# Optimization experiments

Measured on AMD Instinct MI355X. Metric: run time of the kernel, lower is better.

## Reference

```python
import jax, jax.numpy as jnp
import numpy as np

N, E, F0, H = 100000, 3200000, 256, 128
TEMP = 2.0
ALPHA = 0.2  # leaky relu slope
EPS_BN = 1e-5
EPS_LN = 1e-5


def spmm(vals, row, col, X):
    # sparse [N,N] @ dense [N,D] via gather + segment_sum
    return jax.ops.segment_sum(vals[:, None] * X[col], row, num_segments=N)


def batchnorm(h, g, b):
    mu = jnp.mean(h, axis=0, keepdims=True)
    var = jnp.var(h, axis=0, keepdims=True)
    return (h - mu) * jax.lax.rsqrt(var + EPS_BN) * g + b


def layernorm(h, g, b):
    mu = jnp.mean(h, axis=-1, keepdims=True)
    var = jnp.var(h, axis=-1, keepdims=True)
    return (h - mu) * jax.lax.rsqrt(var + EPS_LN) * g + b


def setup_inputs() -> dict:
    key = jax.random.key(0)
    ks = jax.random.split(key, 32)
    x = jax.random.normal(ks[0], (N, F0), dtype=jnp.float32)
    edge_row = jax.random.randint(ks[1], (E,), 0, N)
    edge_col = jax.random.randint(ks[2], (E,), 0, N)
    adj_vals = jax.random.uniform(ks[3], (E,), dtype=jnp.float32) / 32.0  # ~normalized adj
    sf = lambda k, sh: jax.random.normal(k, sh, dtype=jnp.float32) * 0.05
    in_dim = 3 * F0 + 1
    return {
        "x": x, "edge_row": edge_row, "edge_col": edge_col, "adj_vals": adj_vals,
        # LowPassExtractor (GCN)
        "W_gc1": sf(ks[4], (F0, 2 * H)), "b_gc1": jnp.zeros((2 * H,), jnp.float32),
        "bn1_g": jnp.ones((2 * H,), jnp.float32), "bn1_b": jnp.zeros((2 * H,), jnp.float32),
        "W_gc2": sf(ks[5], (2 * H, H)), "b_gc2": jnp.zeros((H,), jnp.float32),
        "bn2_g": jnp.ones((H,), jnp.float32), "bn2_b": jnp.zeros((H,), jnp.float32),
        # Gating
        "Wg1": sf(ks[6], (in_dim, H)), "bg1": jnp.zeros((H,), jnp.float32),
        "ln_g": jnp.ones((H,), jnp.float32), "ln_b": jnp.zeros((H,), jnp.float32),
        "Wg2": sf(ks[7], (H, 2)), "bg2": jnp.zeros((2,), jnp.float32),
        # HighPassExpert
        "Wxp": sf(ks[8], (F0, H)), "bxp": jnp.zeros((H,), jnp.float32),
        "res_scale": jnp.asarray(1.0, jnp.float32),
        "rn_g": jnp.ones((H,), jnp.float32), "rn_b": jnp.zeros((H,), jnp.float32),
        "Wq": sf(ks[9], (H, H)), "Wk": sf(ks[10], (H, H)), "Wv": sf(ks[11], (H, H)),
    }


def reference(x, edge_row, edge_col, adj_vals,
              W_gc1, b_gc1, bn1_g, bn1_b, W_gc2, b_gc2, bn2_g, bn2_b,
              Wg1, bg1, ln_g, ln_b, Wg2, bg2,
              Wxp, bxp, res_scale, rn_g, rn_b, Wq, Wk, Wv):
    # ---- LowPassExtractor: two GCN layers (spmm(adj, xW)+b) with batchnorm+relu
    h1 = jax.nn.relu(batchnorm(spmm(adj_vals, edge_row, edge_col, x @ W_gc1) + b_gc1, bn1_g, bn1_b))
    low = jax.nn.relu(batchnorm(spmm(adj_vals, edge_row, edge_col, h1 @ W_gc2) + b_gc2, bn2_g, bn2_b))

    # ---- Gating: neighborhood stats via spmm
    AX = spmm(adj_vals, edge_row, edge_col, x)
    deg = jax.ops.segment_sum(adj_vals, edge_row, num_segments=N)[:, None]
    x_mean = AX / (deg + 1e-8)
    AX2 = spmm(adj_vals, edge_row, edge_col, x * x)
    var = AX2 / (deg + 1e-8) - x_mean * x_mean
    x_std = jnp.sqrt(jnp.clip(var, 0.0))
    x_cat = jnp.concatenate([x, AX - x, x_std, deg], axis=1)  # [N, 3*F0+1]
    hg = jax.nn.relu(layernorm(x_cat @ Wg1 + bg1, ln_g, ln_b))
    gate = jax.nn.softmax((hg @ Wg2 + bg2) / TEMP, axis=1)  # [N, 2]

    # ---- HighPassExpert: GAT-style sparse attention on normalized residual
    residual = layernorm(res_scale * (x @ Wxp + bxp - low), rn_g, rn_b)
    Q, K, V = residual @ Wq, residual @ Wk, residual @ Wv
    scores = jnp.sum(Q[edge_row] * K[edge_col], axis=1) / jnp.sqrt(jnp.float32(H))
    exp_s = jnp.exp(jnp.where(scores > 0, scores, ALPHA * scores))
    denom = jax.ops.segment_sum(exp_s, edge_row, num_segments=N)
    attn = exp_s / (denom[edge_row] + 1e-16)
    high = jax.ops.segment_sum(attn[:, None] * V[edge_col], edge_row, num_segments=N)

    output = gate[:, 0:1] * low + gate[:, 1:2] * high
    return output, gate, low, high
```

## Files before the change

kernel.cpp:

```cpp
#include <hip/hip_runtime.h>

#define F0 256
#define HD 128
#define NP 100352

typedef unsigned short u16;
typedef __attribute__((ext_vector_type(8))) short short8;
typedef __attribute__((ext_vector_type(4))) float f32x4;

__device__ inline float bf2f(u16 u) {
    union { unsigned int i; float f; } v; v.i = ((unsigned int)u) << 16; return v.f;
}
__device__ inline u16 f2bf(float f) {
    union { float f; unsigned int i; } v; v.f = f;
    unsigned int r = v.i + 0x7FFF + ((v.i >> 16) & 1);
    return (u16)(r >> 16);
}

#define GLOAD16(gp, lp) __builtin_amdgcn_global_load_lds( \
    (const __attribute__((address_space(1))) void*)(gp), \
    (__attribute__((address_space(3))) void*)(lp), 16, 0, 0)

__global__ void k_hist(const int* __restrict__ row, int* __restrict__ counts, int E) {
    int e = blockIdx.x * blockDim.x + threadIdx.x;
    if (e < E) atomicAdd(&counts[row[e]], 1);
}

__global__ void k_scan_blk(const int* __restrict__ counts, int* __restrict__ scan_out,
                           int* __restrict__ partials, int n) {
    __shared__ int wsum[16];
    int t = threadIdx.x;
    int i = blockIdx.x * 1024 + t;
    int v = (i < n) ? counts[i] : 0;
    int lane = t & 63, w = t >> 6;
    #pragma unroll
    for (int off = 1; off < 64; off <<= 1) { int u = __shfl_up(v, off); if (lane >= off) v += u; }
    if (lane == 63) wsum[w] = v;
    __syncthreads();
    if (t < 16) {
        int s = wsum[t];
        #pragma unroll
        for (int off = 1; off < 16; off <<= 1) { int u = __shfl_up(s, off); if (t >= off) s += u; }
        wsum[t] = s;
    }
    __syncthreads();
    int add = (w > 0) ? wsum[w - 1] : 0;
    if (i < n) scan_out[i] = v + add;
    if (t == 1023) partials[blockIdx.x] = wsum[15];
}

__global__ void k_scan_part(int* partials, int nb) {
    __shared__ int ws2[2];
    int t = threadIdx.x;
    int v = (t < nb) ? partials[t] : 0;
    int lane = t & 63, w = t >> 6;
    #pragma unroll
    for (int off = 1; off < 64; off <<= 1) { int u = __shfl_up(v, off); if (lane >= off) v += u; }
    if (lane == 63) ws2[w] = v;
    __syncthreads();
    if (w == 1) v += ws2[0];
    if (t < nb) partials[t] = v;
}

__global__ void k_scan_add(int* __restrict__ row_ptr, const int* __restrict__ partials, int n) {
    int b = blockIdx.x;
    int i = b * 1024 + threadIdx.x;
    if (b == 0 && threadIdx.x == 0) row_ptr[0] = 0;
    int add = (b > 0) ? partials[b - 1] : 0;
    if (i < n) row_ptr[1 + i] += add;
}

__global__ void k_binit(const int* __restrict__ row_ptr, int* __restrict__ bcursor, int nb) {
    int b = blockIdx.x * 256 + threadIdx.x;
    if (b < nb) bcursor[b] = row_ptr[b << 10];
}

__global__ __launch_bounds__(256) void k_bucketA(const int* __restrict__ erow,
                                                 const int* __restrict__ ecol,
                                                 const float* __restrict__ avals,
                                                 int* __restrict__ bcursor,
                                                 int4* __restrict__ tmp, int E, int nb) {
    __shared__ int hcnt[128];
    __shared__ int hbase[128];
    int t = threadIdx.x;
    for (int i = t; i < nb; i += 256) hcnt[i] = 0;
    __syncthreads();
    int start = blockIdx.x * 2048;
    int r[8], c[8]; float v[8]; int loc[8];
    #pragma unroll
    for (int k = 0; k < 8; ++k) {
        int e = start + k * 256 + t;
        bool ok = e < E;
        r[k] = ok ? erow[e] : -1;
        c[k] = ok ? ecol[e] : 0;
        v[k] = ok ? avals[e] : 0.f;
        loc[k] = (r[k] >= 0) ? atomicAdd(&hcnt[r[k] >> 10], 1) : 0;
    }
    __syncthreads();
    for (int i = t; i < nb; i += 256) hbase[i] = atomicAdd(&bcursor[i], hcnt[i]);
    __syncthreads();
    #pragma unroll
    for (int k = 0; k < 8; ++k) {
        if (r[k] >= 0) {
            int b = r[k] >> 10;
            tmp[(size_t)hbase[b] + loc[k]] = make_int4(r[k], c[k], __float_as_int(v[k]), 0);
        }
    }
}

__global__ void k_bucketB(const int4* __restrict__ tmp, const int* __restrict__ row_ptr,
                          int* __restrict__ cursor, int2* __restrict__ cv, int E) {
    for (int e = blockIdx.x * 256 + threadIdx.x; e < E; e += gridDim.x * 256) {
        int4 tt = tmp[e];
        int pos = row_ptr[tt.x] + atomicAdd(&cursor[tt.x], 1);
        cv[pos] = make_int2(tt.y, tt.z);
    }
}

__global__ void k_cast_x(const float* __restrict__ x, u16* __restrict__ xb, int total4) {
    int i = blockIdx.x * blockDim.x + threadIdx.x;
    if (i >= total4) return;
    float4 v = ((const float4*)x)[i];
    ((ushort4*)xb)[i] = make_ushort4(f2bf(v.x), f2bf(v.y), f2bf(v.z), f2bf(v.w));
}

__global__ void k_prep_w(const float* __restrict__ W_gc1, const float* __restrict__ W_gc2,
                         const float* __restrict__ Wg1, const float* __restrict__ Wxp,
                         const float* __restrict__ Wq, const float* __restrict__ Wk,
                         const float* __restrict__ Wv,
                         u16* Wgc1t, u16* Wgc2t, u16* Wdt, u16* W1t, u16* W2t,
                         u16* Wxpt, u16* Wqt, u16* Wkt, u16* Wvt) {
    int z = blockIdx.z;
    int idx = blockIdx.x * 256 + threadIdx.x;
    if (z == 0) { if (idx < 65536) { int n = idx >> 8, k = idx & 255; Wgc1t[idx] = f2bf(W_gc1[k * 256 + n]); } }
    else if (z == 1) { if (idx < 32768) { int n = idx >> 8, k = idx & 255; Wgc2t[idx] = f2bf(W_gc2[k * 128 + n]); } }
    else if (z == 2) { if (idx < 32768) { int n = idx >> 8, k = idx & 255; Wdt[idx] = f2bf(Wg1[k * 128 + n] - Wg1[(k + 256) * 128 + n]); } }
    else if (z == 3) { if (idx < 32768) { int n = idx >> 8, k = idx & 255; W1t[idx] = f2bf(Wg1[(k + 256) * 128 + n]); } }
    else if (z == 4) { if (idx < 32768) { int n = idx >> 8, k = idx & 255; W2t[idx] = f2bf(Wg1[(k + 512) * 128 + n]); } }
    else if (z == 5) { if (idx < 32768) { int n = idx >> 8, k = idx & 255; Wxpt[idx] = f2bf(Wxp[k * 128 + n]); } }
    else if (z == 6) { if (idx < 16384) { int n = idx >> 7, k = idx & 127; Wqt[idx] = f2bf(Wq[k * 128 + n]); } }
    else if (z == 7) { if (idx < 16384) { int n = idx >> 7, k = idx & 127; Wkt[idx] = f2bf(Wk[k * 128 + n]); } }
    else if (z == 8) { if (idx < 16384) { int n = idx >> 7, k = idx & 127; Wvt[idx] = f2bf(Wv[k * 128 + n]); } }
}

__global__ void k_spmm_x2(const u16* __restrict__ Xb, const int* __restrict__ row_ptr,
                          const int2* __restrict__ cv,
                          u16* __restrict__ AXb, u16* __restrict__ XSTDb,
                          float* __restrict__ deg, int N) {
    int wid = blockIdx.x * 4 + (threadIdx.x >> 6);
    if (wid >= N) return;
    int lane = threadIdx.x & 63;
    float a0 = 0, a1 = 0, a2 = 0, a3 = 0;
    float q0 = 0, q1 = 0, q2 = 0, q3 = 0, d = 0;
    int s = row_ptr[wid], e = row_ptr[wid + 1];
    int j = s;
    for (; j + 3 < e; j += 4) {
        int2 cc[4]; ushort4 xb[4];
        #pragma unroll
        for (int t = 0; t < 4; ++t) cc[t] = cv[j + t];
        #pragma unroll
        for (int t = 0; t < 4; ++t) xb[t] = *(const ushort4*)(Xb + (size_t)cc[t].x * F0 + lane * 4);
        #pragma unroll
        for (int t = 0; t < 4; ++t) {
            float x0 = bf2f(xb[t].x), x1 = bf2f(xb[t].y), x2 = bf2f(xb[t].z), x3 = bf2f(xb[t].w);
            float vv = __int_as_float(cc[t].y);
            a0 += vv * x0; a1 += vv * x1; a2 += vv * x2; a3 += vv * x3;
            q0 += vv * x0 * x0; q1 += vv * x1 * x1; q2 += vv * x2 * x2; q3 += vv * x3 * x3;
            d += vv;
        }
    }
    for (; j < e; ++j) {
        int2 cc = cv[j];
        float v0 = __int_as_float(cc.y);
        ushort4 xb0 = *(const ushort4*)(Xb + (size_t)cc.x * F0 + lane * 4);
        float x0 = bf2f(xb0.x), x1 = bf2f(xb0.y), x2 = bf2f(xb0.z), x3 = bf2f(xb0.w);
        a0 += v0 * x0; a1 += v0 * x1; a2 += v0 * x2; a3 += v0 * x3;
        q0 += v0 * x0 * x0; q1 += v0 * x1 * x1; q2 += v0 * x2 * x2; q3 += v0 * x3 * x3;
        d += v0;
    }
    float inv = 1.0f / (d + 1e-8f);
    float m0 = a0 * inv, m1 = a1 * inv, m2 = a2 * inv, m3 = a3 * inv;
    float s0 = sqrtf(fmaxf(q0 * inv - m0 * m0, 0.f));
    float s1 = sqrtf(fmaxf(q1 * inv - m1 * m1, 0.f));
    float s2 = sqrtf(fmaxf(q2 * inv - m2 * m2, 0.f));
    float s3 = sqrtf(fmaxf(q3 * inv - m3 * m3, 0.f));
    *(ushort4*)(AXb + (size_t)wid * F0 + lane * 4) = make_ushort4(f2bf(a0), f2bf(a1), f2bf(a2), f2bf(a3));
    *(ushort4*)(XSTDb + (size_t)wid * F0 + lane * 4) = make_ushort4(f2bf(s0), f2bf(s1), f2bf(s2), f2bf(s3));
    if (lane == 0) deg[wid] = d;
}

__global__ void k_spmm128(const u16* __restrict__ Xb, const int* __restrict__ row_ptr,
                          const int2* __restrict__ cv, u16* __restrict__ OUT, int N) {
    int wid = blockIdx.x * 4 + (threadIdx.x >> 6);
    if (wid >= N) return;
    int lane = threadIdx.x & 63;
    float a0 = 0, a1 = 0;
    int s = row_ptr[wid], e = row_ptr[wid + 1];
    int j = s;
    for (; j + 3 < e; j += 4) {
        int2 cc[4]; ushort2 xb[4];
        #pragma unroll
        for (int t = 0; t < 4; ++t) cc[t] = cv[j + t];
        #pragma unroll
        for (int t = 0; t < 4; ++t) xb[t] = *(const ushort2*)(Xb + (size_t)cc[t].x * HD + lane * 2);
        #pragma unroll
        for (int t = 0; t < 4; ++t) {
            float vv = __int_as_float(cc[t].y);
            a0 += vv * bf2f(xb[t].x); a1 += vv * bf2f(xb[t].y);
        }
    }
    for (; j < e; ++j) {
        int2 cc = cv[j];
        float v0 = __int_as_float(cc.y);
        ushort2 x0 = *(const ushort2*)(Xb + (size_t)cc.x * HD + lane * 2);
        a0 += v0 * bf2f(x0.x); a1 += v0 * bf2f(x0.y);
    }
    *(ushort2*)(OUT + (size_t)wid * HD + lane * 2) = make_ushort2(f2bf(a0), f2bf(a1));
}

__device__ inline void mm_core(const u16* __restrict__ A, const u16* __restrict__ Bt,
                               int K, int ldA, int ldB, int m0, int n0,
                               u16* As, u16* Bs, f32x4 acc[4][4]) {
    int t = threadIdx.x, w = t >> 6, l = t & 63;
    int wr = (w >> 1) * 64, wc = (w & 1) * 64;
    int aoff = (wr + (l & 15)) * 32 + (l >> 4) * 8;
    int boff = (wc + (l & 15)) * 32 + (l >> 4) * 8;
    for (int k0 = 0; k0 < K; k0 += 32) {
        __syncthreads();
        #pragma unroll
        for (int s = 0; s < 2; ++s) {
            int i = s * 256 + t;
            int row = i >> 2, ch = i & 3;
            GLOAD16(A + (size_t)(m0 + row) * ldA + k0 + ch * 8, As + i * 8);
            GLOAD16(Bt + (size_t)(n0 + row) * ldB + k0 + ch * 8, Bs + i * 8);
        }
        __syncthreads();
        short8 af[4], bfr[4];
        #pragma unroll
        for (int i = 0; i < 4; ++i) af[i] = *(const short8*)(As + aoff + i * 16 * 32);
        #pragma unroll
        for (int j = 0; j < 4; ++j) bfr[j] = *(const short8*)(Bs + boff + j * 16 * 32);
        #pragma unroll
        for (int i = 0; i < 4; ++i)
            #pragma unroll
            for (int j = 0; j < 4; ++j)
                acc[i][j] = __builtin_amdgcn_mfma_f32_16x16x32_bf16(af[i], bfr[j], acc[i][j], 0, 0, 0);
    }
}

__device__ inline void mm_zero(f32x4 acc[4][4]) {
    #pragma unroll
    for (int i = 0; i < 4; ++i)
        #pragma unroll
        for (int j = 0; j < 4; ++j)
            acc[i][j] = (f32x4){0.f, 0.f, 0.f, 0.f};
}

__global__ __launch_bounds__(256) void k_mm_f32(const u16* __restrict__ A, const u16* __restrict__ Bt,
                                                float* __restrict__ C, const float* __restrict__ bias,
                                                int M, int K, int Nc) {
    __shared__ __align__(16) u16 As[128 * 32];
    __shared__ __align__(16) u16 Bs[128 * 32];
    int m0 = blockIdx.x * 128, n0 = blockIdx.y * 128;
    f32x4 acc[4][4]; mm_zero(acc);
    mm_core(A, Bt, K, K, K, m0, n0, As, Bs, acc);
    int t = threadIdx.x, w = t >> 6, l = t & 63;
    int rbase = m0 + (w >> 1) * 64 + (l >> 4) * 4;
    int cbase = n0 + (w & 1) * 64 + (l & 15);
    #pragma unroll
    for (int j = 0; j < 4; ++j) {
        float bj = bias ? bias[cbase + j * 16] : 0.f;
        #pragma unroll
        for (int i = 0; i < 4; ++i)
            #pragma unroll
            for (int r = 0; r < 4; ++r) {
                int row = rbase + i * 16 + r;
                if (row < M) C[(size_t)row * Nc + cbase + j * 16] = acc[i][j][r] + bj;
            }
    }
}

__global__ __launch_bounds__(256) void k_mm_bf(const u16* __restrict__ A, const u16* __restrict__ Bt,
                                               u16* __restrict__ C, int M, int K, int Nc) {
    __shared__ __align__(16) u16 As[128 * 32];
    __shared__ __align__(16) u16 Bs[128 * 32];
    int m0 = blockIdx.x * 128, n0 = blockIdx.y * 128;
    f32x4 acc[4][4]; mm_zero(acc);
    mm_core(A, Bt, K, K, K, m0, n0, As, Bs, acc);
    int t = threadIdx.x, w = t >> 6, l = t & 63;
    int rbase = m0 + (w >> 1) * 64 + (l >> 4) * 4;
    int cbase = n0 + (w & 1) * 64 + (l & 15);
    #pragma unroll
    for (int j = 0; j < 4; ++j)
        #pragma unroll
        for (int i = 0; i < 4; ++i)
            #pragma unroll
            for (int r = 0; r < 4; ++r) {
                int row = rbase + i * 16 + r;
                if (row < M) C[(size_t)row * Nc + cbase + j * 16] = f2bf(acc[i][j][r]);
            }
}

__global__ __launch_bounds__(256) void k_mm_gate(const u16* A0, const u16* A1, const u16* A2,
                                                 const u16* B0, const u16* B1, const u16* B2,
                                                 float* __restrict__ C, const float* __restrict__ bg1,
                                                 const float* __restrict__ wlast,
                                                 const float* __restrict__ deg, int M) {
    __shared__ __align__(16) u16 As[128 * 32];
    __shared__ __align__(16) u16 Bs[128 * 32];
    int m0 = blockIdx.x * 128;
    f32x4 acc[4][4]; mm_zero(acc);
    mm_core(A0, B0, 256, 256, 256, m0, 0, As, Bs, acc);
    mm_core(A1, B1, 256, 256, 256, m0, 0, As, Bs, acc);
    mm_core(A2, B2, 256, 256, 256, m0, 0, As, Bs, acc);
    int t = threadIdx.x, w = t >> 6, l = t & 63;
    int rbase = m0 + (w >> 1) * 64 + (l >> 4) * 4;
    int cbase = (w & 1) * 64 + (l & 15);
    float wl[4], bg[4];
    #pragma unroll
    for (int j = 0; j < 4; ++j) { wl[j] = wlast[cbase + j * 16]; bg[j] = bg1[cbase + j * 16]; }
    float dg[4][4];
    #pragma unroll
    for (int i = 0; i < 4; ++i)
        #pragma unroll
        for (int r = 0; r < 4; ++r) {
            int row = rbase + i * 16 + r;
            dg[i][r] = (row < M) ? deg[row] : 0.f;
        }
    #pragma unroll
    for (int j = 0; j < 4; ++j)
        #pragma unroll
        for (int i = 0; i < 4; ++i)
            #pragma unroll
            for (int r = 0; r < 4; ++r) {
                int row = rbase + i * 16 + r;
                if (row < M) C[(size_t)row * 128 + cbase + j * 16] = acc[i][j][r] + bg[j] + dg[i][r] * wl[j];
            }
}

__global__ __launch_bounds__(256) void k_mm_qkv(const u16* __restrict__ A,
                                                const u16* Wqt, const u16* Wkt, const u16* Wvt,
                                                float* Q, u16* Kb, u16* Vb, int M) {
    __shared__ __align__(16) u16 As[128 * 32];
    __shared__ __align__(16) u16 Bs[128 * 32];
    int z = blockIdx.z;
    const u16* Bt = (z == 0) ? Wqt : (z == 1) ? Wkt : Wvt;
    int m0 = blockIdx.x * 128;
    f32x4 acc[4][4]; mm_zero(acc);
    mm_core(A, Bt, 128, 128, 128, m0, 0, As, Bs, acc);
    int t = threadIdx.x, w = t >> 6, l = t & 63;
    int rbase = m0 + (w >> 1) * 64 + (l >> 4) * 4;
    int cbase = (w & 1) * 64 + (l & 15);
    if (z == 0) {
        #pragma unroll
        for (int j = 0; j < 4; ++j)
            #pragma unroll
            for (int i = 0; i < 4; ++i)
                #pragma unroll
                for (int r = 0; r < 4; ++r) {
                    int row = rbase + i * 16 + r;
                    if (row < M) Q[(size_t)row * 128 + cbase + j * 16] = acc[i][j][r];
                }
    } else {
        u16* C = (z == 1) ? Kb : Vb;
        #pragma unroll
        for (int j = 0; j < 4; ++j)
            #pragma unroll
            for (int i = 0; i < 4; ++i)
                #pragma unroll
                for (int r = 0; r < 4; ++r) {
                    int row = rbase + i * 16 + r;
                    if (row < M) C[(size_t)row * 128 + cbase + j * 16] = f2bf(acc[i][j][r]);
                }
    }
}

__global__ void k_bn_stats_bf(const u16* __restrict__ H, double* __restrict__ stats, int N, int C) {
    int t = threadIdx.x;
    int rpt = 256 / C;
    int rsub = t / C;
    int col = t - rsub * C;
    double s = 0.0, q = 0.0;
    for (long r = (long)blockIdx.x * rpt + rsub; r < N; r += (long)gridDim.x * rpt) {
        float v = bf2f(H[(size_t)r * C + col]);
        s += v; q += (double)v * v;
    }
    __shared__ double sh_s[256], sh_q[256];
    sh_s[t] = s; sh_q[t] = q;
    __syncthreads();
    if (t < C) {
        for (int k = 1; k < rpt; ++k) { s += sh_s[t + k * C]; q += sh_q[t + k * C]; }
        atomicAdd(&stats[t], s);
        atomicAdd(&stats[C + t], q);
    }
}

__global__ void k_bn_fin(const double* __restrict__ stats, const float* __restrict__ g,
                         const float* __restrict__ b, float* __restrict__ scale,
                         float* __restrict__ shift, int C, double invN) {
    int t = threadIdx.x;
    if (t >= C) return;
    double mean = stats[t] * invN;
    double var = stats[C + t] * invN - mean * mean;
    float sc = (float)((double)g[t] / sqrt(var + 1e-5));
    scale[t] = sc;
    shift[t] = b[t] - (float)mean * sc;
}

__global__ void k_bn_relu_bb(const u16* __restrict__ in, u16* __restrict__ out,
                             const float* __restrict__ scale, const float* __restrict__ shift,
                             int total4, int cmask4) {
    int i = blockIdx.x * blockDim.x + threadIdx.x;
    if (i >= total4) return;
    int c4 = i & cmask4;
    ushort4 v = ((const ushort4*)in)[i];
    float4 sc = ((const float4*)scale)[c4];
    float4 sh = ((const float4*)shift)[c4];
    ((ushort4*)out)[i] = make_ushort4(
        f2bf(fmaxf(bf2f(v.x) * sc.x + sh.x, 0.f)), f2bf(fmaxf(bf2f(v.y) * sc.y + sh.y, 0.f)),
        f2bf(fmaxf(bf2f(v.z) * sc.z + sh.z, 0.f)), f2bf(fmaxf(bf2f(v.w) * sc.w + sh.w, 0.f)));
}

__global__ void k_bn_relu_bf(const u16* __restrict__ in, float* __restrict__ out,
                             const float* __restrict__ scale, const float* __restrict__ shift,
                             int total4, int cmask4) {
    int i = blockIdx.x * blockDim.x + threadIdx.x;
    if (i >= total4) return;
    int c4 = i & cmask4;
    ushort4 v = ((const ushort4*)in)[i];
    float4 sc = ((const float4*)scale)[c4];
    float4 sh = ((const float4*)shift)[c4];
    ((float4*)out)[i] = make_float4(
        fmaxf(bf2f(v.x) * sc.x + sh.x, 0.f), fmaxf(bf2f(v.y) * sc.y + sh.y, 0.f),
        fmaxf(bf2f(v.z) * sc.z + sh.z, 0.f), fmaxf(bf2f(v.w) * sc.w + sh.w, 0.f));
}

__global__ void k_ln_gate(const float* __restrict__ Hg, const float* __restrict__ g,
                          const float* __restrict__ b, const float* __restrict__ Wg2,
                          const float* __restrict__ bg2, float* __restrict__ gate, int N) {
    int wid = blockIdx.x * 4 + (threadIdx.x >> 6);
    if (wid >= N) return;
    int lane = threadIdx.x & 63;
    float2 h = *(const float2*)(Hg + (size_t)wid * HD + lane * 2);
    float s1 = h.x + h.y, s2 = h.x * h.x + h.y * h.y;
    #pragma unroll
    for (int off = 32; off > 0; off >>= 1) { s1 += __shfl_xor(s1, off); s2 += __shfl_xor(s2, off); }
    float mu = s1 * (1.f / 128.f);
    float var = s2 * (1.f / 128.f) - mu * mu;
    float is = 1.0f / sqrtf(var + 1e-5f);
    float2 gg = *(const float2*)(g + lane * 2);
    float2 bb = *(const float2*)(b + lane * 2);
    float y0 = fmaxf((h.x - mu) * is * gg.x + bb.x, 0.f);
    float y1 = fmaxf((h.y - mu) * is * gg.y + bb.y, 0.f);
    float4 w = ((const float4*)Wg2)[lane];
    float t0 = y0 * w.x + y1 * w.z;
    float t1 = y0 * w.y + y1 * w.w;
    #pragma unroll
    for (int off = 32; off > 0; off >>= 1) { t0 += __shfl_xor(t0, off); t1 += __shfl_xor(t1, off); }
    if (lane == 0) {
        t0 = (t0 + bg2[0]) * 0.5f;
        t1 = (t1 + bg2[1]) * 0.5f;
        float m = fmaxf(t0, t1);
        float e0 = __expf(t0 - m), e1 = __expf(t1 - m);
        float inv = 1.0f / (e0 + e1);
        gate[(size_t)wid * 2 + 0] = e0 * inv;
        gate[(size_t)wid * 2 + 1] = e1 * inv;
    }
}

__global__ void k_resid_ln(const float* __restrict__ R0, const float* __restrict__ low,
                           const float* __restrict__ g, const float* __restrict__ b,
                           const float* __restrict__ rs_ptr, u16* __restrict__ resid, int N) {
    int wid = blockIdx.x * 4 + (threadIdx.x >> 6);
    if (wid >= N) return;
    int lane = threadIdx.x & 63;
    float rs = rs_ptr[0];
    float2 a = *(const float2*)(R0 + (size_t)wid * HD + lane * 2);
    float2 l = *(const float2*)(low + (size_t)wid * HD + lane * 2);
    float h0 = rs * (a.x - l.x), h1 = rs * (a.y - l.y);
    float s1 = h0 + h1, s2 = h0 * h0 + h1 * h1;
    #pragma unroll
    for (int off = 32; off > 0; off >>= 1) { s1 += __shfl_xor(s1, off); s2 += __shfl_xor(s2, off); }
    float mu = s1 * (1.f / 128.f);
    float var = s2 * (1.f / 128.f) - mu * mu;
    float is = 1.0f / sqrtf(var + 1e-5f);
    float2 gg = *(const float2*)(g + lane * 2);
    float2 bb = *(const float2*)(b + lane * 2);
    float y0 = (h0 - mu) * is * gg.x + bb.x;
    float y1 = (h1 - mu) * is * gg.y + bb.y;
    *(ushort2*)(resid + (size_t)wid * HD + lane * 2) = make_ushort2(f2bf(y0), f2bf(y1));
}

__global__ void k_attn_aggr(const float* __restrict__ Q, const u16* __restrict__ Kb,
                            const u16* __restrict__ Vb, const int* __restrict__ row_ptr,
                            const int2* __restrict__ cv,
                            const float* __restrict__ gate, const float* __restrict__ low,
                            float* __restrict__ high, float* __restrict__ outp, int N) {
    int wid = blockIdx.x * 4 + (threadIdx.x >> 6);
    if (wid >= N) return;
    int lane = threadIdx.x & 63;
    int sub = lane & 15;
    int g = lane >> 4;
    float qs[8];
    {
        const float4* qp = (const float4*)(Q + (size_t)wid * HD + sub * 8);
        float4 q0 = qp[0], q1 = qp[1];
        qs[0] = q0.x; qs[1] = q0.y; qs[2] = q0.z; qs[3] = q0.w;
        qs[4] = q1.x; qs[5] = q1.y; qs[6] = q1.z; qs[7] = q1.w;
    }
    float2 qv = *(const float2*)(Q + (size_t)wid * HD + lane * 2);
    float n0 = 0, n1 = 0, den = 0;
    int s = row_ptr[wid], e = row_ptr[wid + 1];
    int j = s;
    for (; j + 3 < e; j += 4) {
        int cg = cv[j + g].x;
        short8 kk = *(const short8*)(Kb + (size_t)cg * HD + sub * 8);
        float p = qs[0] * bf2f((u16)kk[0]) + qs[1] * bf2f((u16)kk[1])
                + qs[2] * bf2f((u16)kk[2]) + qs[3] * bf2f((u16)kk[3])
                + qs[4] * bf2f((u16)kk[4]) + qs[5] * bf2f((u16)kk[5])
                + qs[6] * bf2f((u16)kk[6]) + qs[7] * bf2f((u16)kk[7]);
        p += __shfl_xor(p, 1); p += __shfl_xor(p, 2);
        p += __shfl_xor(p, 4); p += __shfl_xor(p, 8);
        float sc = p * 0.08838834764831845f;
        float ls = sc > 0.f ? sc : 0.2f * sc;
        float ex = __expf(ls);
        float exb[4]; int cb[4];
        #pragma unroll
        for (int t = 0; t < 4; ++t) { exb[t] = __shfl(ex, t << 4); cb[t] = __shfl(cg, t << 4); }
        ushort2 vb[4];
        #pragma unroll
        for (int t = 0; t < 4; ++t) vb[t] = *(const ushort2*)(Vb + (size_t)cb[t] * HD + lane * 2);
        #pragma unroll
        for (int t = 0; t < 4; ++t) {
            n0 += exb[t] * bf2f(vb[t].x);
            n1 += exb[t] * bf2f(vb[t].y);
            den += exb[t];
        }
    }
    for (; j < e; ++j) {
        int c0 = cv[j].x;
        ushort2 kb0 = *(const ushort2*)(Kb + (size_t)c0 * HD + lane * 2);
        ushort2 vb0 = *(const ushort2*)(Vb + (size_t)c0 * HD + lane * 2);
        float sc0 = qv.x * bf2f(kb0.x) + qv.y * bf2f(kb0.y);
        #pragma unroll
        for (int off = 32; off > 0; off >>= 1) sc0 += __shfl_xor(sc0, off);
        float p = sc0 * 0.08838834764831845f;
        float ls = p > 0.f ? p : 0.2f * p;
        float ex = __expf(ls);
        n0 += ex * bf2f(vb0.x); n1 += ex * bf2f(vb0.y); den += ex;
    }
    float inv = 1.0f / (den + 1e-16f);
    float h0 = n0 * inv, h1 = n1 * inv;
    *(float2*)(high + (size_t)wid * HD + lane * 2) = make_float2(h0, h1);
    float g0 = gate[(size_t)wid * 2 + 0], g1 = gate[(size_t)wid * 2 + 1];
    float2 lw = *(const float2*)(low + (size_t)wid * HD + lane * 2);
    *(float2*)(outp + (size_t)wid * HD + lane * 2) = make_float2(g0 * lw.x + g1 * h0, g0 * lw.y + g1 * h1);
}

extern "C" void kernel_launch(void* const* d_in, const int* in_sizes, int n_in,
                              void* d_out, int out_size, void* d_ws, size_t ws_size,
                              hipStream_t stream) {
    const float* x      = (const float*)d_in[0];
    const int*   erow   = (const int*)d_in[1];
    const int*   ecol   = (const int*)d_in[2];
    const float* avals  = (const float*)d_in[3];
    const float* W_gc1  = (const float*)d_in[4];
    const float* bn1_g  = (const float*)d_in[6];
    const float* bn1_b  = (const float*)d_in[7];
    const float* W_gc2  = (const float*)d_in[8];
    const float* bn2_g  = (const float*)d_in[10];
    const float* bn2_b  = (const float*)d_in[11];
    const float* Wg1    = (const float*)d_in[12];
    const float* bg1    = (const float*)d_in[13];
    const float* ln_g   = (const float*)d_in[14];
    const float* ln_b   = (const float*)d_in[15];
    const float* Wg2    = (const float*)d_in[16];
    const float* bg2    = (const float*)d_in[17];
    const float* Wxp    = (const float*)d_in[18];
    const float* bxp    = (const float*)d_in[19];
    const float* rscale = (const float*)d_in[20];
    const float* rn_g   = (const float*)d_in[21];
    const float* rn_b   = (const float*)d_in[22];
    const float* Wq     = (const float*)d_in[23];
    const float* Wk     = (const float*)d_in[24];
    const float* Wv     = (const float*)d_in[25];

    const int N = in_sizes[0] / F0;
    const int E = in_sizes[1];

    char* base = (char*)d_ws;
    size_t off = 0;
    auto carve = [&](size_t bytes) -> char* {
        char* p = base + off;
        off += (bytes + 255) & ~(size_t)255;
        return p;
    };
    double* stats  = (double*)carve(4096);
    float* scaleb  = (float*)carve(1024);
    float* shiftb  = (float*)carve(1024);
    int*   partials= (int*)carve(2048);
    int*   bcursor = (int*)carve(512);
    u16* Wgc1t = (u16*)carve(65536 * 2);
    u16* Wgc2t = (u16*)carve(32768 * 2);
    u16* Wdt   = (u16*)carve(32768 * 2);
    u16* W1t   = (u16*)carve(32768 * 2);
    u16* W2t   = (u16*)carve(32768 * 2);
    u16* Wxpt  = (u16*)carve(32768 * 2);
    u16* Wqt   = (u16*)carve(16384 * 2);
    u16* Wkt   = (u16*)carve(16384 * 2);
    u16* Wvt   = (u16*)carve(16384 * 2);
    int*   row_ptr = (int*)carve((size_t)(N + 1) * 4);
    int*   cursor  = (int*)carve((size_t)N * 4);
    float* deg     = (float*)carve((size_t)N * 4);
    int2*  cv      = (int2*)carve((size_t)E * 8);
    u16*   x_bf    = (u16*)carve((size_t)NP * F0 * 2);
    u16*   kvb     = (u16*)carve((size_t)NP * HD * 2 * 2);
    u16*   AX_bf   = (u16*)carve((size_t)NP * F0 * 2);
    u16*   XSTD_bf = (u16*)carve((size_t)NP * F0 * 2);
    u16*   h1_bf   = (u16*)carve((size_t)NP * F0 * 2);
    float* BIG3    = (float*)carve((size_t)NP * HD * 4);
    u16*   G2_bf   = (u16*)carve((size_t)NP * HD * 2);
    float* M3      = (float*)carve((size_t)NP * HD * 4);
    (void)ws_size; (void)n_in; (void)out_size;

    u16*   Kb    = kvb;
    u16*   Vb    = kvb + (size_t)N * HD;
    u16*   S1_bf = h1_bf;
    u16*   S2_bf = (u16*)BIG3;
    u16*   resid_bf = h1_bf;
    int4*  tmp   = (int4*)M3;

    float* out_o    = (float*)d_out;
    float* out_gate = out_o + (size_t)N * HD;
    float* out_low  = out_gate + (size_t)N * 2;
    float* out_high = out_low + (size_t)N * HD;

    const int eb  = (E + 255) / 256;
    const int wb  = (N + 3) / 4;
    const int NB1 = (N + 1023) / 1024;
    const int nb  = (N + 1023) >> 10;
    const int gx  = (N + 127) / 128;
    const dim3 blk(256);

    hipMemsetAsync(cursor, 0, (size_t)N * 4, stream);
    k_hist<<<eb, blk, 0, stream>>>(erow, cursor, E);
    k_scan_blk<<<NB1, 1024, 0, stream>>>(cursor, row_ptr + 1, partials, N);
    k_scan_part<<<1, 128, 0, stream>>>(partials, NB1);
    k_scan_add<<<NB1, 1024, 0, stream>>>(row_ptr, partials, N);
    k_binit<<<1, blk, 0, stream>>>(row_ptr, bcursor, nb);
    k_bucketA<<<(E + 2047) / 2048, blk, 0, stream>>>(erow, ecol, avals, bcursor, tmp, E, nb);
    hipMemsetAsync(cursor, 0, (size_t)N * 4, stream);
    k_bucketB<<<2048, blk, 0, stream>>>(tmp, row_ptr, cursor, cv, E);

    k_cast_x<<<(N * 64 + 255) / 256, blk, 0, stream>>>(x, x_bf, N * 64);
    k_prep_w<<<dim3(256, 1, 9), blk, 0, stream>>>(W_gc1, W_gc2, Wg1, Wxp, Wq, Wk, Wv,
                                                  Wgc1t, Wgc2t, Wdt, W1t, W2t, Wxpt, Wqt, Wkt, Wvt);

    k_spmm_x2<<<wb, blk, 0, stream>>>(x_bf, row_ptr, cv, AX_bf, XSTD_bf, deg, N);

    k_mm_bf<<<dim3(gx, 2), blk, 0, stream>>>(AX_bf, Wgc1t, S1_bf, N, 256, 256);
    hipMemsetAsync(stats, 0, 4096, stream);
    k_bn_stats_bf<<<1024, blk, 0, stream>>>(S1_bf, stats, N, 256);
    k_bn_fin<<<1, blk, 0, stream>>>(stats, bn1_g, bn1_b, scaleb, shiftb, 256, 1.0 / N);
    k_bn_relu_bb<<<(N * 64 + 255) / 256, blk, 0, stream>>>(S1_bf, h1_bf, scaleb, shiftb, N * 64, 63);
    k_mm_bf<<<dim3(gx, 1), blk, 0, stream>>>(h1_bf, Wgc2t, G2_bf, N, 256, 128);
    k_spmm128<<<wb, blk, 0, stream>>>(G2_bf, row_ptr, cv, S2_bf, N);
    hipMemsetAsync(stats, 0, 2048, stream);
    k_bn_stats_bf<<<1024, blk, 0, stream>>>(S2_bf, stats, N, 128);
    k_bn_fin<<<1, blk, 0, stream>>>(stats, bn2_g, bn2_b, scaleb, shiftb, 128, 1.0 / N);
    k_bn_relu_bf<<<(N * 32 + 255) / 256, blk, 0, stream>>>(S2_bf, out_low, scaleb, shiftb, N * 32, 31);

    k_mm_gate<<<dim3(gx, 1), blk, 0, stream>>>(x_bf, AX_bf, XSTD_bf, Wdt, W1t, W2t,
                                               M3, bg1, Wg1 + (size_t)768 * 128, deg, N);
    k_ln_gate<<<wb, blk, 0, stream>>>(M3, ln_g, ln_b, Wg2, bg2, out_gate, N);

    k_mm_f32<<<dim3(gx, 1), blk, 0, stream>>>(x_bf, Wxpt, BIG3, bxp, N, 256, 128);
    k_resid_ln<<<wb, blk, 0, stream>>>(BIG3, out_low, rn_g, rn_b, rscale, resid_bf, N);
    k_mm_qkv<<<dim3(gx, 1, 3), blk, 0, stream>>>(resid_bf, Wqt, Wkt, Wvt, M3, Kb, Vb, N);
    k_attn_aggr<<<wb, blk, 0, stream>>>(M3, Kb, Vb, row_ptr, cv, out_gate, out_low, out_high, out_o, N);
}
```

Baseline: 1.549 ms.

## Simplify CSR build via atomic ranks, unroll gathers by 8, interleave K/V

The histogram kernel now records each edge's atomic rank, so a single direct scatter kernel replaces the two-pass bucketed CSR construction and its extra memset. The SpMM and attention-aggregation kernels add an 8-edge unrolled loop to keep more gathers in flight. K and V are stored interleaved per node in one 256-wide row, so both come from the same region of memory. The direct scatter writes to random positions in cv, losing the locality that bucketing provided, and the wider unroll raises register pressure.

```diff
diff --git a/kernel.cpp b/kernel.cpp
--- a/kernel.cpp
+++ b/kernel.cpp
@@ -21,9 +21,10 @@
     (const __attribute__((address_space(1))) void*)(gp), \
     (__attribute__((address_space(3))) void*)(lp), 16, 0, 0)
 
-__global__ void k_hist(const int* __restrict__ row, int* __restrict__ counts, int E) {
+__global__ void k_hist_rank(const int* __restrict__ row, int* __restrict__ counts,
+                            int* __restrict__ rank, int E) {
     int e = blockIdx.x * blockDim.x + threadIdx.x;
-    if (e < E) atomicAdd(&counts[row[e]], 1);
+    if (e < E) rank[e] = atomicAdd(&counts[row[e]], 1);
 }
 
 __global__ void k_scan_blk(const int* __restrict__ counts, int* __restrict__ scan_out,
@@ -70,51 +71,14 @@
     if (i < n) row_ptr[1 + i] += add;
 }
 
-__global__ void k_binit(const int* __restrict__ row_ptr, int* __restrict__ bcursor, int nb) {
-    int b = blockIdx.x * 256 + threadIdx.x;
-    if (b < nb) bcursor[b] = row_ptr[b << 10];
-}
-
-__global__ __launch_bounds__(256) void k_bucketA(const int* __restrict__ erow,
-                                                 const int* __restrict__ ecol,
-                                                 const float* __restrict__ avals,
-                                                 int* __restrict__ bcursor,
-                                                 int4* __restrict__ tmp, int E, int nb) {
-    __shared__ int hcnt[128];
-    __shared__ int hbase[128];
-    int t = threadIdx.x;
-    for (int i = t; i < nb; i += 256) hcnt[i] = 0;
-    __syncthreads();
-    int start = blockIdx.x * 2048;
-    int r[8], c[8]; float v[8]; int loc[8];
-    #pragma unroll
-    for (int k = 0; k < 8; ++k) {
-        int e = start + k * 256 + t;
-        bool ok = e < E;
-        r[k] = ok ? erow[e] : -1;
-        c[k] = ok ? ecol[e] : 0;
-        v[k] = ok ? avals[e] : 0.f;
-        loc[k] = (r[k] >= 0) ? atomicAdd(&hcnt[r[k] >> 10], 1) : 0;
-    }
-    __syncthreads();
-    for (int i = t; i < nb; i += 256) hbase[i] = atomicAdd(&bcursor[i], hcnt[i]);
-    __syncthreads();
-    #pragma unroll
-    for (int k = 0; k < 8; ++k) {
-        if (r[k] >= 0) {
-            int b = r[k] >> 10;
-            tmp[(size_t)hbase[b] + loc[k]] = make_int4(r[k], c[k], __float_as_int(v[k]), 0);
-        }
-    }
-}
-
-__global__ void k_bucketB(const int4* __restrict__ tmp, const int* __restrict__ row_ptr,
-                          int* __restrict__ cursor, int2* __restrict__ cv, int E) {
-    for (int e = blockIdx.x * 256 + threadIdx.x; e < E; e += gridDim.x * 256) {
-        int4 tt = tmp[e];
-        int pos = row_ptr[tt.x] + atomicAdd(&cursor[tt.x], 1);
-        cv[pos] = make_int2(tt.y, tt.z);
-    }
+__global__ void k_scatter_direct(const int* __restrict__ row, const int* __restrict__ ecol,
+                                 const float* __restrict__ avals, const int* __restrict__ rank,
+                                 const int* __restrict__ row_ptr, int2* __restrict__ cv, int E) {
+    int e = blockIdx.x * blockDim.x + threadIdx.x;
+    if (e >= E) return;
+    int r = row[e];
+    int pos = row_ptr[r] + rank[e];
+    cv[pos] = make_int2(ecol[e], __float_as_int(avals[e]));
 }
 
 __global__ void k_cast_x(const float* __restrict__ x, u16* __restrict__ xb, int total4) {
@@ -154,6 +118,21 @@
     float q0 = 0, q1 = 0, q2 = 0, q3 = 0, d = 0;
     int s = row_ptr[wid], e = row_ptr[wid + 1];
     int j = s;
+    for (; j + 7 < e; j += 8) {
+        int2 cc[8]; ushort4 xb[8];
+        #pragma unroll
+        for (int t = 0; t < 8; ++t) cc[t] = cv[j + t];
+        #pragma unroll
+        for (int t = 0; t < 8; ++t) xb[t] = *(const ushort4*)(Xb + (size_t)cc[t].x * F0 + lane * 4);
+        #pragma unroll
+        for (int t = 0; t < 8; ++t) {
+            float x0 = bf2f(xb[t].x), x1 = bf2f(xb[t].y), x2 = bf2f(xb[t].z), x3 = bf2f(xb[t].w);
+            float vv = __int_as_float(cc[t].y);
+            a0 += vv * x0; a1 += vv * x1; a2 += vv * x2; a3 += vv * x3;
+            q0 += vv * x0 * x0; q1 += vv * x1 * x1; q2 += vv * x2 * x2; q3 += vv * x3 * x3;
+            d += vv;
+        }
+    }
     for (; j + 3 < e; j += 4) {
         int2 cc[4]; ushort4 xb[4];
         #pragma unroll
@@ -197,6 +176,18 @@
     float a0 = 0, a1 = 0;
     int s = row_ptr[wid], e = row_ptr[wid + 1];
     int j = s;
+    for (; j + 7 < e; j += 8) {
+        int2 cc[8]; ushort2 xb[8];
+        #pragma unroll
+        for (int t = 0; t < 8; ++t) cc[t] = cv[j + t];
+        #pragma unroll
+        for (int t = 0; t < 8; ++t) xb[t] = *(const ushort2*)(Xb + (size_t)cc[t].x * HD + lane * 2);
+        #pragma unroll
+        for (int t = 0; t < 8; ++t) {
+            float vv = __int_as_float(cc[t].y);
+            a0 += vv * bf2f(xb[t].x); a1 += vv * bf2f(xb[t].y);
+        }
+    }
     for (; j + 3 < e; j += 4) {
         int2 cc[4]; ushort2 xb[4];
         #pragma unroll
@@ -340,7 +331,7 @@
 
 __global__ __launch_bounds__(256) void k_mm_qkv(const u16* __restrict__ A,
                                                 const u16* Wqt, const u16* Wkt, const u16* Wvt,
-                                                float* Q, u16* Kb, u16* Vb, int M) {
+                                                float* Q, u16* KV, int M) {
     __shared__ __align__(16) u16 As[128 * 32];
     __shared__ __align__(16) u16 Bs[128 * 32];
     int z = blockIdx.z;
@@ -362,7 +353,7 @@
                     if (row < M) Q[(size_t)row * 128 + cbase + j * 16] = acc[i][j][r];
                 }
     } else {
-        u16* C = (z == 1) ? Kb : Vb;
+        int coff = (z == 1) ? 0 : 128;
         #pragma unroll
         for (int j = 0; j < 4; ++j)
             #pragma unroll
@@ -370,7 +361,7 @@
                 #pragma unroll
                 for (int r = 0; r < 4; ++r) {
                     int row = rbase + i * 16 + r;
-                    if (row < M) C[(size_t)row * 128 + cbase + j * 16] = f2bf(acc[i][j][r]);
+                    if (row < M) KV[(size_t)row * 256 + coff + cbase + j * 16] = f2bf(acc[i][j][r]);
                 }
     }
 }
@@ -491,9 +482,8 @@
     *(ushort2*)(resid + (size_t)wid * HD + lane * 2) = make_ushort2(f2bf(y0), f2bf(y1));
 }
 
-__global__ void k_attn_aggr(const float* __restrict__ Q, const u16* __restrict__ Kb,
-                            const u16* __restrict__ Vb, const int* __restrict__ row_ptr,
-                            const int2* __restrict__ cv,
+__global__ void k_attn_aggr(const float* __restrict__ Q, const u16* __restrict__ KV,
+                            const int* __restrict__ row_ptr, const int2* __restrict__ cv,
                             const float* __restrict__ gate, const float* __restrict__ low,
                             float* __restrict__ high, float* __restrict__ outp, int N) {
     int wid = blockIdx.x * 4 + (threadIdx.x >> 6);
@@ -512,9 +502,48 @@
     float n0 = 0, n1 = 0, den = 0;
     int s = row_ptr[wid], e = row_ptr[wid + 1];
     int j = s;
+    for (; j + 7 < e; j += 8) {
+        int cg0 = cv[j + g].x;
+        int cg1 = cv[j + 4 + g].x;
+        short8 ka = *(const short8*)(KV + (size_t)cg0 * 256 + sub * 8);
+        short8 kb = *(const short8*)(KV + (size_t)cg1 * 256 + sub * 8);
+        float p0 = qs[0] * bf2f((u16)ka[0]) + qs[1] * bf2f((u16)ka[1])
+                 + qs[2] * bf2f((u16)ka[2]) + qs[3] * bf2f((u16)ka[3])
+                 + qs[4] * bf2f((u16)ka[4]) + qs[5] * bf2f((u16)ka[5])
+                 + qs[6] * bf2f((u16)ka[6]) + qs[7] * bf2f((u16)ka[7]);
+        float p1 = qs[0] * bf2f((u16)kb[0]) + qs[1] * bf2f((u16)kb[1])
+                 + qs[2] * bf2f((u16)kb[2]) + qs[3] * bf2f((u16)kb[3])
+                 + qs[4] * bf2f((u16)kb[4]) + qs[5] * bf2f((u16)kb[5])
+                 + qs[6] * bf2f((u16)kb[6]) + qs[7] * bf2f((u16)kb[7]);
+        p0 += __shfl_xor(p0, 1); p1 += __shfl_xor(p1, 1);
+        p0 += __shfl_xor(p0, 2); p1 += __shfl_xor(p1, 2);
+        p0 += __shfl_xor(p0, 4); p1 += __shfl_xor(p1, 4);
+        p0 += __shfl_xor(p0, 8); p1 += __shfl_xor(p1, 8);
+        float sc0 = p0 * 0.08838834764831845f;
+        float sc1 = p1 * 0.08838834764831845f;
+        float ls0 = sc0 > 0.f ? sc0 : 0.2f * sc0;
+        float ls1 = sc1 > 0.f ? sc1 : 0.2f * sc1;
+        float ex0 = __expf(ls0);
+        float ex1 = __expf(ls1);
+        float exb[8]; int cb[8];
+        #pragma unroll
+        for (int t = 0; t < 4; ++t) {
+            exb[t]     = __shfl(ex0, t << 4); cb[t]     = __shfl(cg0, t << 4);
+            exb[4 + t] = __shfl(ex1, t << 4); cb[4 + t] = __shfl(cg1, t << 4);
+        }
+        ushort2 vb[8];
+        #pragma unroll
+        for (int t = 0; t < 8; ++t) vb[t] = *(const ushort2*)(KV + (size_t)cb[t] * 256 + 128 + lane * 2);
+        #pragma unroll
+        for (int t = 0; t < 8; ++t) {
+            n0 += exb[t] * bf2f(vb[t].x);
+            n1 += exb[t] * bf2f(vb[t].y);
+            den += exb[t];
+        }
+    }
     for (; j + 3 < e; j += 4) {
         int cg = cv[j + g].x;
-        short8 kk = *(const short8*)(Kb + (size_t)cg * HD + sub * 8);
+        short8 kk = *(const short8*)(KV + (size_t)cg * 256 + sub * 8);
         float p = qs[0] * bf2f((u16)kk[0]) + qs[1] * bf2f((u16)kk[1])
                 + qs[2] * bf2f((u16)kk[2]) + qs[3] * bf2f((u16)kk[3])
                 + qs[4] * bf2f((u16)kk[4]) + qs[5] * bf2f((u16)kk[5])
@@ -529,7 +558,7 @@
         for (int t = 0; t < 4; ++t) { exb[t] = __shfl(ex, t << 4); cb[t] = __shfl(cg, t << 4); }
         ushort2 vb[4];
         #pragma unroll
-        for (int t = 0; t < 4; ++t) vb[t] = *(const ushort2*)(Vb + (size_t)cb[t] * HD + lane * 2);
+        for (int t = 0; t < 4; ++t) vb[t] = *(const ushort2*)(KV + (size_t)cb[t] * 256 + 128 + lane * 2);
         #pragma unroll
         for (int t = 0; t < 4; ++t) {
             n0 += exb[t] * bf2f(vb[t].x);
@@ -539,8 +568,8 @@
     }
     for (; j < e; ++j) {
         int c0 = cv[j].x;
-        ushort2 kb0 = *(const ushort2*)(Kb + (size_t)c0 * HD + lane * 2);
-        ushort2 vb0 = *(const ushort2*)(Vb + (size_t)c0 * HD + lane * 2);
+        ushort2 kb0 = *(const ushort2*)(KV + (size_t)c0 * 256 + lane * 2);
+        ushort2 vb0 = *(const ushort2*)(KV + (size_t)c0 * 256 + 128 + lane * 2);
         float sc0 = qv.x * bf2f(kb0.x) + qv.y * bf2f(kb0.y);
         #pragma unroll
         for (int off = 32; off > 0; off >>= 1) sc0 += __shfl_xor(sc0, off);
@@ -599,7 +628,6 @@
     float* scaleb  = (float*)carve(1024);
     float* shiftb  = (float*)carve(1024);
     int*   partials= (int*)carve(2048);
-    int*   bcursor = (int*)carve(512);
     u16* Wgc1t = (u16*)carve(65536 * 2);
     u16* Wgc2t = (u16*)carve(32768 * 2);
     u16* Wdt   = (u16*)carve(32768 * 2);
@@ -614,7 +642,7 @@
     float* deg     = (float*)carve((size_t)N * 4);
     int2*  cv      = (int2*)carve((size_t)E * 8);
     u16*   x_bf    = (u16*)carve((size_t)NP * F0 * 2);
-    u16*   kvb     = (u16*)carve((size_t)NP * HD * 2 * 2);
+    u16*   kvb     = (u16*)carve((size_t)NP * 256 * 2);
     u16*   AX_bf   = (u16*)carve((size_t)NP * F0 * 2);
     u16*   XSTD_bf = (u16*)carve((size_t)NP * F0 * 2);
     u16*   h1_bf   = (u16*)carve((size_t)NP * F0 * 2);
@@ -623,12 +651,10 @@
     float* M3      = (float*)carve((size_t)NP * HD * 4);
     (void)ws_size; (void)n_in; (void)out_size;
 
-    u16*   Kb    = kvb;
-    u16*   Vb    = kvb + (size_t)N * HD;
     u16*   S1_bf = h1_bf;
     u16*   S2_bf = (u16*)BIG3;
     u16*   resid_bf = h1_bf;
-    int4*  tmp   = (int4*)M3;
+    int*   rank  = (int*)M3;
 
     float* out_o    = (float*)d_out;
     float* out_gate = out_o + (size_t)N * HD;
@@ -638,19 +664,15 @@
     const int eb  = (E + 255) / 256;
     const int wb  = (N + 3) / 4;
     const int NB1 = (N + 1023) / 1024;
-    const int nb  = (N + 1023) >> 10;
     const int gx  = (N + 127) / 128;
     const dim3 blk(256);
 
     hipMemsetAsync(cursor, 0, (size_t)N * 4, stream);
-    k_hist<<<eb, blk, 0, stream>>>(erow, cursor, E);
+    k_hist_rank<<<eb, blk, 0, stream>>>(erow, cursor, rank, E);
     k_scan_blk<<<NB1, 1024, 0, stream>>>(cursor, row_ptr + 1, partials, N);
     k_scan_part<<<1, 128, 0, stream>>>(partials, NB1);
     k_scan_add<<<NB1, 1024, 0, stream>>>(row_ptr, partials, N);
-    k_binit<<<1, blk, 0, stream>>>(row_ptr, bcursor, nb);
-    k_bucketA<<<(E + 2047) / 2048, blk, 0, stream>>>(erow, ecol, avals, bcursor, tmp, E, nb);
-    hipMemsetAsync(cursor, 0, (size_t)N * 4, stream);
-    k_bucketB<<<2048, blk, 0, stream>>>(tmp, row_ptr, cursor, cv, E);
+    k_scatter_direct<<<eb, blk, 0, stream>>>(erow, ecol, avals, rank, row_ptr, cv, E);
 
     k_cast_x<<<(N * 64 + 255) / 256, blk, 0, stream>>>(x, x_bf, N * 64);
     k_prep_w<<<dim3(256, 1, 9), blk, 0, stream>>>(W_gc1, W_gc2, Wg1, Wxp, Wq, Wk, Wv,
@@ -676,6 +698,6 @@
 
     k_mm_f32<<<dim3(gx, 1), blk, 0, stream>>>(x_bf, Wxpt, BIG3, bxp, N, 256, 128);
     k_resid_ln<<<wb, blk, 0, stream>>>(BIG3, out_low, rn_g, rn_b, rscale, resid_bf, N);
-    k_mm_qkv<<<dim3(gx, 1, 3), blk, 0, stream>>>(resid_bf, Wqt, Wkt, Wvt, M3, Kb, Vb, N);
-    k_attn_aggr<<<wb, blk, 0, stream>>>(M3, Kb, Vb, row_ptr, cv, out_gate, out_low, out_high, out_o, N);
-}
+    k_mm_qkv<<<dim3(gx, 1, 3), blk, 0, stream>>>(resid_bf, Wqt, Wkt, Wvt, M3, kvb, N);
+    k_attn_aggr<<<wb, blk, 0, stream>>>(M3, kvb, row_ptr, cv, out_gate, out_low, out_high, out_o, N);
+}
```

Result: faster. 1.458 ms (-5.9%).
